# Performance work log

Measured on AMD Instinct MI355X. Metric: run time of the kernel, lower is better.

Reference implementation:

```python
import jax, jax.numpy as jnp
import numpy as np

B, TQ, TK, E, H, DH = 4, 1024, 1024, 1024, 16, 64
EPS = 1e-5

def setup_inputs() -> dict:
    key = jax.random.key(0)
    ks = jax.random.split(key, 16)
    s = 0.02
    return {
        "x": jax.random.normal(ks[0], (B, TQ, E), jnp.float32),
        "encoder_out": jax.random.normal(ks[1], (B, TK, E), jnp.float32),
        "Q1w": jax.random.normal(ks[2], (H, DH, E), jnp.float32) * s,
        "Q1b": jax.random.normal(ks[3], (H, DH), jnp.float32) * s,
        "Q2w": jax.random.normal(ks[4], (H, DH, E), jnp.float32) * s,
        "Q2b": jax.random.normal(ks[5], (H, DH), jnp.float32) * s,
        "K1w": jax.random.normal(ks[6], (H, DH, E), jnp.float32) * s,
        "K1b": jax.random.normal(ks[7], (H, DH), jnp.float32) * s,
        "K2w": jax.random.normal(ks[8], (H, DH, E), jnp.float32) * s,
        "K2b": jax.random.normal(ks[9], (H, DH), jnp.float32) * s,
        "Vw": jax.random.normal(ks[10], (H, DH, E), jnp.float32) * s,
        "Vb": jax.random.normal(ks[11], (H, DH), jnp.float32) * s,
        "lam": jax.random.uniform(ks[12], (H,), jnp.float32, 0.5, 1.0),
        "gn_gamma": jnp.ones((H * DH,), jnp.float32),
        "gn_beta": jnp.zeros((H * DH,), jnp.float32),
        "out_w": jax.random.normal(ks[13], (E, H * DH), jnp.float32) * s,
        "out_b": jax.random.normal(ks[14], (E,), jnp.float32) * s,
    }

def _proj(inp, w, b):
    # inp: [B,T,E], w: [H,DH,E] -> [B,H,T,DH]
    return jnp.einsum('bte,hde->bhtd', inp, w) + b[None, :, None, :]

def reference(x, encoder_out, Q1w, Q1b, Q2w, Q2b, K1w, K1b, K2w, K2b, Vw, Vb,
              lam, gn_gamma, gn_beta, out_w, out_b):
    scale = 1.0 / jnp.sqrt(jnp.float32(DH))
    q1 = _proj(x, Q1w, Q1b)
    q2 = _proj(x, Q2w, Q2b)
    k1 = _proj(encoder_out, K1w, K1b)
    k2 = _proj(encoder_out, K2w, K2b)
    v = _proj(encoder_out, Vw, Vb)
    s1 = jnp.einsum('bhtd,bhsd->bhts', q1, k1) * scale  # [B,H,TQ,TK]
    s2 = jnp.einsum('bhtd,bhsd->bhts', q2, k2) * scale
    w = jax.nn.softmax(s1, axis=-1) - lam[None, :, None, None] * jax.nn.softmax(s2, axis=-1)
    out = jnp.einsum('bhts,bhsd->bhtd', w, v)  # [B,H,TQ,DH]
    # GroupNorm(num_groups=H, channels=H*DH) over [B,C,T]: per (B,H) stats over (T,DH)
    mu = jnp.mean(out, axis=(2, 3), keepdims=True)
    var = jnp.mean(jnp.square(out - mu), axis=(2, 3), keepdims=True)
    normed = (out - mu) * jax.lax.rsqrt(var + EPS)
    g = gn_gamma.reshape(H, DH)[None, :, None, :]
    b_ = gn_beta.reshape(H, DH)[None, :, None, :]
    normed = normed * g + b_
    y = normed.transpose(0, 2, 1, 3).reshape(B, TQ, H * DH)
    return y @ out_w.T + out_b
```

## Files before the change

kernel.cpp:

```cpp
#include <hip/hip_runtime.h>
#include <cmath>

typedef __bf16 bf16_t;
typedef bf16_t bf16x8 __attribute__((ext_vector_type(8)));
typedef bf16_t bf16x4 __attribute__((ext_vector_type(4)));
typedef float  f32x4  __attribute__((ext_vector_type(4)));

#define Bn  4
#define TQn 1024
#define TKn 1024
#define En  1024
#define Hn  16
#define DHn 64

static constexpr float EPSv = 1e-5f;
static constexpr float C_SCALE = 0.18033688011112042f;

#define GLDS16(g, l)                                                         \
    __builtin_amdgcn_global_load_lds(                                        \
        (const __attribute__((address_space(1))) void*)(g),                  \
        (__attribute__((address_space(3))) void*)(l), 16, 0, 0)

__global__ __launch_bounds__(256)
void cvt_all(const float* __restrict__ x, const float* __restrict__ enc,
             const float* __restrict__ q1w, const float* __restrict__ q2w,
             const float* __restrict__ k1w, const float* __restrict__ k2w,
             const float* __restrict__ vw,  const float* __restrict__ outw,
             bf16_t* __restrict__ xb, bf16_t* __restrict__ encb,
             bf16_t* __restrict__ wq, bf16_t* __restrict__ wkv,
             bf16_t* __restrict__ wob, float* __restrict__ stats)
{
    if (blockIdx.x == 0 && threadIdx.x < 128) stats[threadIdx.x] = 0.f;
    int idx = blockIdx.x * 256 + threadIdx.x;
    const float* src; bf16_t* dst;
    if      (idx < 1048576) { src = x    + (size_t)idx * 4;              dst = xb   + (size_t)idx * 4; }
    else if (idx < 2097152) { src = enc  + (size_t)(idx - 1048576) * 4;  dst = encb + (size_t)(idx - 1048576) * 4; }
    else if (idx < 2359296) { src = q1w  + (size_t)(idx - 2097152) * 4;  dst = wq   + (size_t)(idx - 2097152) * 4; }
    else if (idx < 2621440) { src = q2w  + (size_t)(idx - 2359296) * 4;  dst = wq   + 1048576 + (size_t)(idx - 2359296) * 4; }
    else if (idx < 2883584) { src = k1w  + (size_t)(idx - 2621440) * 4;  dst = wkv  + (size_t)(idx - 2621440) * 4; }
    else if (idx < 3145728) { src = k2w  + (size_t)(idx - 2883584) * 4;  dst = wkv  + 1048576 + (size_t)(idx - 2883584) * 4; }
    else if (idx < 3407872) { src = vw   + (size_t)(idx - 3145728) * 4;  dst = wkv  + 2097152 + (size_t)(idx - 3145728) * 4; }
    else                    { src = outw + (size_t)(idx - 3407872) * 4;  dst = wob  + (size_t)(idx - 3407872) * 4; }
    float4 v = *(const float4*)src;
    bf16x4 o;
    o[0] = (bf16_t)v.x; o[1] = (bf16_t)v.y; o[2] = (bf16_t)v.z; o[3] = (bf16_t)v.w;
    *(bf16x4*)dst = o;
}

template<int OUTMODE>
__global__ __launch_bounds__(256, 3)
void gemm_bf16(const bf16_t* __restrict__ A, const bf16_t* __restrict__ W,
               const float* __restrict__ b0, const float* __restrict__ b1,
               const float* __restrict__ b2, void* __restrict__ Cout, int K)
{
    __shared__ bf16_t sA[128 * 64];
    __shared__ bf16_t sB[128 * 64];
    const int tid = threadIdx.x;
    const int w = tid >> 6, lane = tid & 63;
    const int q = lane >> 4, r = lane & 15;
    const int wm = w & 1, wn = w >> 1;
    const int blockM = blockIdx.y * 128, blockN = blockIdx.x * 128;

    f32x4 acc[4][4];
#pragma unroll
    for (int i = 0; i < 4; ++i)
#pragma unroll
        for (int j = 0; j < 4; ++j) acc[i][j] = (f32x4){0.f, 0.f, 0.f, 0.f};

    for (int k0 = 0; k0 < K; k0 += 64) {
#pragma unroll
        for (int c = 0; c < 4; ++c) {
            const int s = c * 256 + tid;
            const int row = s >> 3;
            const int cg = (s & 7) ^ (row & 7);
            GLDS16(A + (size_t)(blockM + row) * K + k0 + cg * 8, sA + c * 2048 + w * 512);
            GLDS16(W + (size_t)(blockN + row) * K + k0 + cg * 8, sB + c * 2048 + w * 512);
        }
        __syncthreads();
#pragma unroll
        for (int ks = 0; ks < 2; ++ks) {
            bf16x8 a[4], b[4];
#pragma unroll
            for (int i = 0; i < 4; ++i) {
                const int row = wm * 64 + i * 16 + r;
                const int g = (ks * 4 + q) ^ (row & 7);
                a[i] = *(const bf16x8*)&sA[row * 64 + g * 8];
            }
#pragma unroll
            for (int j = 0; j < 4; ++j) {
                const int row = wn * 64 + j * 16 + r;
                const int g = (ks * 4 + q) ^ (row & 7);
                b[j] = *(const bf16x8*)&sB[row * 64 + g * 8];
            }
#pragma unroll
            for (int i = 0; i < 4; ++i)
#pragma unroll
                for (int j = 0; j < 4; ++j)
                    acc[i][j] = __builtin_amdgcn_mfma_f32_16x16x32_bf16(a[i], b[j], acc[i][j], 0, 0, 0);
        }
        __syncthreads();
    }

    const int seg = blockN >> 10;
    const float* bp = (seg == 0) ? b0 : ((seg == 1) ? b1 : b2);
#pragma unroll
    for (int j = 0; j < 4; ++j) {
        const int n = blockN + wn * 64 + j * 16 + r;
        const float bv = bp[n & 1023];
#pragma unroll
        for (int i = 0; i < 4; ++i) {
            f32x4 v = acc[i][j];
#pragma unroll
            for (int e = 0; e < 4; ++e) {
                const int m = blockM + wm * 64 + i * 16 + q * 4 + e;
                const float val = v[e] + bv;
                if (OUTMODE == 0) {
                    const int bb = m >> 10, t = m & 1023;
                    const int h = (n >> 6) & 15, d = n & 63;
                    ((bf16_t*)Cout)[((((size_t)seg * 4 + bb) * 16 + h) * 1024 + t) * 64 + d] = (bf16_t)val;
                } else {
                    ((float*)Cout)[(size_t)m * 1024 + n] = val;
                }
            }
        }
    }
}

__device__ __forceinline__ void compute_S(const bf16_t* __restrict__ sK,
                                          const bf16x8 (&fQ)[2][2],
                                          f32x4 (&S)[4][2], int q, int r)
{
#pragma unroll
    for (int i = 0; i < 4; ++i)
#pragma unroll
        for (int j = 0; j < 2; ++j) S[i][j] = (f32x4){0.f, 0.f, 0.f, 0.f};
#pragma unroll
    for (int ks = 0; ks < 2; ++ks) {
        bf16x8 fK[4];
#pragma unroll
        for (int i = 0; i < 4; ++i) {
            const int row = i * 16 + r;
            const int g = (ks * 4 + q) ^ (row & 7);
            fK[i] = *(const bf16x8*)&sK[row * 64 + g * 8];
        }
#pragma unroll
        for (int i = 0; i < 4; ++i)
#pragma unroll
            for (int j = 0; j < 2; ++j)
                S[i][j] = __builtin_amdgcn_mfma_f32_16x16x32_bf16(fK[i], fQ[j][ks], S[i][j], 0, 0, 0);
    }
}

__device__ __forceinline__ void softmax_pw(f32x4 (&S)[4][2], bf16_t* __restrict__ sPt,
                                           float (&l)[2], int w, int q, int r)
{
#pragma unroll
    for (int j = 0; j < 2; ++j) {
        const int t = w * 32 + j * 16 + r;
        float part = 0.f;
#pragma unroll
        for (int i = 0; i < 4; ++i) {
            bf16x4 pk;
#pragma unroll
            for (int e = 0; e < 4; ++e) {
                const float p = __builtin_amdgcn_exp2f(S[i][j][e] * C_SCALE);
                part += p;
                pk[e] = (bf16_t)p;
            }
            const int sb = i * 16 + q * 4;
            const int g = (sb >> 3) ^ (t & 7);
            *(bf16x4*)&sPt[t * 64 + g * 8 + (sb & 7)] = pk;
        }
        l[j] += part;
    }
}

__device__ __forceinline__ void pv(const bf16_t* __restrict__ sPt,
                                   const bf16x8 (&fV)[4][2],
                                   f32x4 (&O)[2][4], int w, int q, int r)
{
#pragma unroll
    for (int ks = 0; ks < 2; ++ks) {
        bf16x8 fP[2];
#pragma unroll
        for (int i2 = 0; i2 < 2; ++i2) {
            const int m = w * 32 + i2 * 16 + r;
            const int g = (ks * 4 + q) ^ (m & 7);
            fP[i2] = *(const bf16x8*)&sPt[m * 64 + g * 8];
        }
#pragma unroll
        for (int i2 = 0; i2 < 2; ++i2)
#pragma unroll
            for (int j = 0; j < 4; ++j)
                O[i2][j] = __builtin_amdgcn_mfma_f32_16x16x32_bf16(fP[i2], fV[j][ks], O[i2][j], 0, 0, 0);
    }
}

__global__ __launch_bounds__(256, 2)
void diff_attn_mfma(const bf16_t* __restrict__ q12, const bf16_t* __restrict__ k12v,
                    const float* __restrict__ lam, bf16_t* __restrict__ out,
                    float* __restrict__ stats)
{
    __shared__ bf16_t sK1[2][64 * 64];
    __shared__ bf16_t sK2[2][64 * 64];
    __shared__ bf16_t sVt[64 * 64];
    __shared__ bf16_t sPt1[128 * 64];
    __shared__ bf16_t sPt2[128 * 64];
    __shared__ float  sl1[128], sl2[128];
    __shared__ float  sred[16];

    const int tid = threadIdx.x;
    const int w = tid >> 6, lane = tid & 63;
    const int q = lane >> 4, r = lane & 15;
    const int bh = blockIdx.x, qt = blockIdx.y;
    const float lamv = lam[bh & (Hn - 1)];

    const size_t HT = (size_t)TKn * DHn;
    const bf16_t* q1g = q12 + (size_t)bh * HT + (size_t)qt * 128 * DHn;
    const bf16_t* q2g = q1g + 64 * HT;
    const bf16_t* k1g = k12v + (size_t)bh * HT;
    const bf16_t* k2g = k1g + 64 * HT;
    const bf16_t* vg  = k1g + 128 * HT;

    bf16x8 fQ1[2][2], fQ2[2][2];
#pragma unroll
    for (int j = 0; j < 2; ++j) {
        const int t = w * 32 + j * 16 + r;
#pragma unroll
        for (int ks = 0; ks < 2; ++ks) {
            fQ1[j][ks] = *(const bf16x8*)(q1g + (size_t)t * 64 + ks * 32 + q * 8);
            fQ2[j][ks] = *(const bf16x8*)(q2g + (size_t)t * 64 + ks * 32 + q * 8);
        }
    }

    f32x4 O1[2][4], O2[2][4];
    float l1[2] = {0.f, 0.f}, l2[2] = {0.f, 0.f};
#pragma unroll
    for (int i = 0; i < 2; ++i)
#pragma unroll
        for (int j = 0; j < 4; ++j) { O1[i][j] = (f32x4){0.f,0.f,0.f,0.f}; O2[i][j] = (f32x4){0.f,0.f,0.f,0.f}; }

    {
#pragma unroll
        for (int c = 0; c < 2; ++c) {
            const int s = c * 256 + tid;
            const int row = s >> 3;
            const int cg = (s & 7) ^ (row & 7);
            GLDS16(k1g + row * 64 + cg * 8, &sK1[0][c * 2048 + w * 512]);
            GLDS16(k2g + row * 64 + cg * 8, &sK2[0][c * 2048 + w * 512]);
        }
        bf16x8 v0[2];
#pragma unroll
        for (int rep = 0; rep < 2; ++rep)
            v0[rep] = *(const bf16x8*)(vg + (size_t)lane * 64 + (w * 2 + rep) * 8);
        __syncthreads();
#pragma unroll
        for (int rep = 0; rep < 2; ++rep) {
            const int d0 = (w * 2 + rep) * 8;
#pragma unroll
            for (int i = 0; i < 8; ++i) {
                const int d = d0 + i;
                sVt[d * 64 + (((lane >> 3) ^ i) << 3) + (lane & 7)] = v0[rep][i];
            }
        }
        __syncthreads();
    }

    bf16x8 vr[2];
    for (int st = 0; st < TKn / 64; ++st) {
        const int cur = st & 1;
        if (st < 15) {
            const bf16_t* k1p = k1g + (size_t)(st + 1) * 4096;
            const bf16_t* k2p = k2g + (size_t)(st + 1) * 4096;
#pragma unroll
            for (int c = 0; c < 2; ++c) {
                const int s = c * 256 + tid;
                const int row = s >> 3;
                const int cg = (s & 7) ^ (row & 7);
                GLDS16(k1p + row * 64 + cg * 8, &sK1[cur ^ 1][c * 2048 + w * 512]);
                GLDS16(k2p + row * 64 + cg * 8, &sK2[cur ^ 1][c * 2048 + w * 512]);
            }
            const bf16_t* vp = vg + (size_t)(st + 1) * 4096;
#pragma unroll
            for (int rep = 0; rep < 2; ++rep)
                vr[rep] = *(const bf16x8*)(vp + (size_t)lane * 64 + (w * 2 + rep) * 8);
        }

        {
            f32x4 S[4][2];
            compute_S(sK1[cur], fQ1, S, q, r);
            softmax_pw(S, sPt1, l1, w, q, r);
        }
        {
            f32x4 S[4][2];
            compute_S(sK2[cur], fQ2, S, q, r);
            softmax_pw(S, sPt2, l2, w, q, r);
        }
        bf16x8 fV[4][2];
#pragma unroll
        for (int j = 0; j < 4; ++j)
#pragma unroll
            for (int ks = 0; ks < 2; ++ks) {
                const int d = j * 16 + r;
                const int g = (ks * 4 + q) ^ (d & 7);
                fV[j][ks] = *(const bf16x8*)&sVt[d * 64 + g * 8];
            }
        pv(sPt1, fV, O1, w, q, r);
        pv(sPt2, fV, O2, w, q, r);

        __syncthreads();
        if (st < 15) {
#pragma unroll
            for (int rep = 0; rep < 2; ++rep) {
                const int d0 = (w * 2 + rep) * 8;
#pragma unroll
                for (int i = 0; i < 8; ++i) {
                    const int d = d0 + i;
                    sVt[d * 64 + (((lane >> 3) ^ i) << 3) + (lane & 7)] = vr[rep][i];
                }
            }
            __syncthreads();
        }
    }

#pragma unroll
    for (int j = 0; j < 2; ++j) {
        float v1 = l1[j];
        v1 += __shfl_xor(v1, 16); v1 += __shfl_xor(v1, 32);
        float v2 = l2[j];
        v2 += __shfl_xor(v2, 16); v2 += __shfl_xor(v2, 32);
        if (q == 0) { sl1[w * 32 + j * 16 + r] = v1; sl2[w * 32 + j * 16 + r] = v2; }
    }

    bf16_t* op = out + ((size_t)bh * TQn + (size_t)qt * 128) * DHn;
    float ssum = 0.f, ssq = 0.f;
#pragma unroll
    for (int i2 = 0; i2 < 2; ++i2)
#pragma unroll
        for (int e = 0; e < 4; ++e) {
            const int t = w * 32 + i2 * 16 + q * 4 + e;
            const float inv1 = 1.0f / sl1[t];
            const float inv2 = lamv / sl2[t];
#pragma unroll
            for (int j = 0; j < 4; ++j) {
                const float o = O1[i2][j][e] * inv1 - O2[i2][j][e] * inv2;
                op[(size_t)t * 64 + j * 16 + r] = (bf16_t)o;
                ssum += o;
                ssq += o * o;
            }
        }
#pragma unroll
    for (int d = 1; d < 64; d <<= 1) {
        ssum += __shfl_xor(ssum, d);
        ssq  += __shfl_xor(ssq, d);
    }
    if (lane == 0) { sred[w] = ssum; sred[8 + w] = ssq; }
    __syncthreads();
    if (tid == 0) {
        atomicAdd(&stats[bh],      sred[0] + sred[1] + sred[2] + sred[3]);
        atomicAdd(&stats[64 + bh], sred[8] + sred[9] + sred[10] + sred[11]);
    }
}

__global__ __launch_bounds__(256)
void gn_apply(const bf16_t* __restrict__ attn, const float* __restrict__ stats,
              const float* __restrict__ gamma, const float* __restrict__ beta,
              bf16_t* __restrict__ y)
{
    const int f = blockIdx.x * 256 + threadIdx.x;
    const int d8 = (f & 7) << 3;
    const int t  = (f >> 3) & 1023;
    const int bh = f >> 13;
    const int h  = bh & 15;
    const int b  = bh >> 4;
    const float s1 = stats[bh], s2 = stats[64 + bh];
    const float mu = s1 * (1.f / 65536.f);
    const float var = s2 * (1.f / 65536.f) - mu * mu;
    const float rstd = rsqrtf(var + EPSv);
    bf16x8 v = *(const bf16x8*)&attn[((size_t)bh << 16) + t * 64 + d8];
    const int c = h * 64 + d8;
    const float* gp = gamma + c;
    const float* bp = beta + c;
    bf16x8 o;
#pragma unroll
    for (int i = 0; i < 8; ++i)
        o[i] = (bf16_t)(((float)v[i] - mu) * rstd * gp[i] + bp[i]);
    *(bf16x8*)&y[((size_t)(b * 1024 + t)) * 1024 + c] = o;
}

extern "C" void kernel_launch(void* const* d_in, const int* in_sizes, int n_in,
                              void* d_out, int out_size, void* d_ws, size_t ws_size,
                              hipStream_t stream)
{
    const float* x    = (const float*)d_in[0];
    const float* enc  = (const float*)d_in[1];
    const float* Q1w  = (const float*)d_in[2];
    const float* Q1b  = (const float*)d_in[3];
    const float* Q2w  = (const float*)d_in[4];
    const float* Q2b  = (const float*)d_in[5];
    const float* K1w  = (const float*)d_in[6];
    const float* K1b  = (const float*)d_in[7];
    const float* K2w  = (const float*)d_in[8];
    const float* K2b  = (const float*)d_in[9];
    const float* Vw   = (const float*)d_in[10];
    const float* Vb   = (const float*)d_in[11];
    const float* lam  = (const float*)d_in[12];
    const float* gng  = (const float*)d_in[13];
    const float* gnb  = (const float*)d_in[14];
    const float* outw = (const float*)d_in[15];
    const float* outb = (const float*)d_in[16];
    float* out = (float*)d_out;

    bf16_t* xb   = (bf16_t*)d_ws;
    bf16_t* encb = xb   + 4194304;
    bf16_t* wq   = encb + 4194304;
    bf16_t* wkv  = wq   + 2097152;
    bf16_t* wob  = wkv  + 3145728;
    bf16_t* q12  = wob  + 1048576;
    bf16_t* k12v = q12  + 8388608;
    bf16_t* yb   = k12v + 12582912;
    bf16_t* attnb= yb   + 4194304;
    float*  stats= (float*)(attnb + 4194304);

    cvt_all<<<14336, 256, 0, stream>>>(x, enc, Q1w, Q2w, K1w, K2w, Vw, outw,
                                       xb, encb, wq, wkv, wob, stats);

    gemm_bf16<0><<<dim3(16, 32), 256, 0, stream>>>(xb,   wq,  Q1b, Q2b, Q2b, q12,  1024);
    gemm_bf16<0><<<dim3(24, 32), 256, 0, stream>>>(encb, wkv, K1b, K2b, Vb,  k12v, 1024);

    diff_attn_mfma<<<dim3(64, 8), 256, 0, stream>>>(q12, k12v, lam, attnb, stats);

    gn_apply<<<2048, 256, 0, stream>>>(attnb, stats, gng, gnb, yb);

    gemm_bf16<1><<<dim3(8, 32), 256, 0, stream>>>(yb, wob, outb, outb, outb, out, 1024);
}
```

Measured before the change: 251.1 us.

## Split attention KV loop across two wave groups and pre-transpose V in GEMM

```diff
diff --git a/kernel.cpp b/kernel.cpp
--- a/kernel.cpp
+++ b/kernel.cpp
@@ -114,10 +114,14 @@
             for (int e = 0; e < 4; ++e) {
                 const int m = blockM + wm * 64 + i * 16 + q * 4 + e;
                 const float val = v[e] + bv;
-                if (OUTMODE == 0) {
+                if (OUTMODE == 0 || OUTMODE == 2) {
                     const int bb = m >> 10, t = m & 1023;
                     const int h = (n >> 6) & 15, d = n & 63;
-                    ((bf16_t*)Cout)[((((size_t)seg * 4 + bb) * 16 + h) * 1024 + t) * 64 + d] = (bf16_t)val;
+                    const size_t base = ((size_t)(seg * 4 + bb) * 16 + h) * 65536;
+                    if (OUTMODE == 2 && seg == 2)
+                        ((bf16_t*)Cout)[base + (size_t)d * 1024 + t] = (bf16_t)val;
+                    else
+                        ((bf16_t*)Cout)[base + (size_t)t * 64 + d] = (bf16_t)val;
                 } else {
                     ((float*)Cout)[(size_t)m * 1024 + n] = val;
                 }
@@ -126,97 +130,27 @@
     }
 }
 
-__device__ __forceinline__ void compute_S(const bf16_t* __restrict__ sK,
-                                          const bf16x8 (&fQ)[2][2],
-                                          f32x4 (&S)[4][2], int q, int r)
-{
-#pragma unroll
-    for (int i = 0; i < 4; ++i)
-#pragma unroll
-        for (int j = 0; j < 2; ++j) S[i][j] = (f32x4){0.f, 0.f, 0.f, 0.f};
-#pragma unroll
-    for (int ks = 0; ks < 2; ++ks) {
-        bf16x8 fK[4];
-#pragma unroll
-        for (int i = 0; i < 4; ++i) {
-            const int row = i * 16 + r;
-            const int g = (ks * 4 + q) ^ (row & 7);
-            fK[i] = *(const bf16x8*)&sK[row * 64 + g * 8];
-        }
-#pragma unroll
-        for (int i = 0; i < 4; ++i)
-#pragma unroll
-            for (int j = 0; j < 2; ++j)
-                S[i][j] = __builtin_amdgcn_mfma_f32_16x16x32_bf16(fK[i], fQ[j][ks], S[i][j], 0, 0, 0);
-    }
-}
-
-__device__ __forceinline__ void softmax_pw(f32x4 (&S)[4][2], bf16_t* __restrict__ sPt,
-                                           float (&l)[2], int w, int q, int r)
-{
-#pragma unroll
-    for (int j = 0; j < 2; ++j) {
-        const int t = w * 32 + j * 16 + r;
-        float part = 0.f;
-#pragma unroll
-        for (int i = 0; i < 4; ++i) {
-            bf16x4 pk;
-#pragma unroll
-            for (int e = 0; e < 4; ++e) {
-                const float p = __builtin_amdgcn_exp2f(S[i][j][e] * C_SCALE);
-                part += p;
-                pk[e] = (bf16_t)p;
-            }
-            const int sb = i * 16 + q * 4;
-            const int g = (sb >> 3) ^ (t & 7);
-            *(bf16x4*)&sPt[t * 64 + g * 8 + (sb & 7)] = pk;
-        }
-        l[j] += part;
-    }
-}
-
-__device__ __forceinline__ void pv(const bf16_t* __restrict__ sPt,
-                                   const bf16x8 (&fV)[4][2],
-                                   f32x4 (&O)[2][4], int w, int q, int r)
-{
-#pragma unroll
-    for (int ks = 0; ks < 2; ++ks) {
-        bf16x8 fP[2];
-#pragma unroll
-        for (int i2 = 0; i2 < 2; ++i2) {
-            const int m = w * 32 + i2 * 16 + r;
-            const int g = (ks * 4 + q) ^ (m & 7);
-            fP[i2] = *(const bf16x8*)&sPt[m * 64 + g * 8];
-        }
-#pragma unroll
-        for (int i2 = 0; i2 < 2; ++i2)
-#pragma unroll
-            for (int j = 0; j < 4; ++j)
-                O[i2][j] = __builtin_amdgcn_mfma_f32_16x16x32_bf16(fP[i2], fV[j][ks], O[i2][j], 0, 0, 0);
-    }
-}
-
-__global__ __launch_bounds__(256, 2)
+__global__ __launch_bounds__(512, 4)
 void diff_attn_mfma(const bf16_t* __restrict__ q12, const bf16_t* __restrict__ k12v,
                     const float* __restrict__ lam, bf16_t* __restrict__ out,
                     float* __restrict__ stats)
 {
-    __shared__ bf16_t sK1[2][64 * 64];
-    __shared__ bf16_t sK2[2][64 * 64];
-    __shared__ bf16_t sVt[64 * 64];
-    __shared__ bf16_t sPt1[128 * 64];
-    __shared__ bf16_t sPt2[128 * 64];
-    __shared__ float  sl1[128], sl2[128];
-    __shared__ float  sred[16];
+    __shared__ __align__(16) bf16_t smem[20480];
 
     const int tid = threadIdx.x;
     const int w = tid >> 6, lane = tid & 63;
+    const int wg = w >> 2, wl = w & 3;
     const int q = lane >> 4, r = lane & 15;
     const int bh = blockIdx.x, qt = blockIdx.y;
     const float lamv = lam[bh & (Hn - 1)];
 
+    bf16_t* sK1 = smem + wg * 2048;
+    bf16_t* sK2 = smem + 4096 + wg * 2048;
+    bf16_t* sVt = smem + 8192 + wg * 2048;
+    bf16_t* sPt = smem + 12288 + w * 1024;
+
     const size_t HT = (size_t)TKn * DHn;
-    const bf16_t* q1g = q12 + (size_t)bh * HT + (size_t)qt * 128 * DHn;
+    const bf16_t* q1g = q12 + (size_t)bh * HT + ((size_t)qt * 128 + wl * 32) * 64;
     const bf16_t* q2g = q1g + 64 * HT;
     const bf16_t* k1g = k12v + (size_t)bh * HT;
     const bf16_t* k2g = k1g + 64 * HT;
@@ -225,11 +159,11 @@
     bf16x8 fQ1[2][2], fQ2[2][2];
 #pragma unroll
     for (int j = 0; j < 2; ++j) {
-        const int t = w * 32 + j * 16 + r;
+        const int t_l = j * 16 + r;
 #pragma unroll
         for (int ks = 0; ks < 2; ++ks) {
-            fQ1[j][ks] = *(const bf16x8*)(q1g + (size_t)t * 64 + ks * 32 + q * 8);
-            fQ2[j][ks] = *(const bf16x8*)(q2g + (size_t)t * 64 + ks * 32 + q * 8);
+            fQ1[j][ks] = *(const bf16x8*)(q1g + (size_t)t_l * 64 + ks * 32 + q * 8);
+            fQ2[j][ks] = *(const bf16x8*)(q2g + (size_t)t_l * 64 + ks * 32 + q * 8);
         }
     }
 
@@ -240,125 +174,157 @@
 #pragma unroll
         for (int j = 0; j < 4; ++j) { O1[i][j] = (f32x4){0.f,0.f,0.f,0.f}; O2[i][j] = (f32x4){0.f,0.f,0.f,0.f}; }
 
-    {
-#pragma unroll
-        for (int c = 0; c < 2; ++c) {
-            const int s = c * 256 + tid;
-            const int row = s >> 3;
-            const int cg = (s & 7) ^ (row & 7);
-            GLDS16(k1g + row * 64 + cg * 8, &sK1[0][c * 2048 + w * 512]);
-            GLDS16(k2g + row * 64 + cg * 8, &sK2[0][c * 2048 + w * 512]);
-        }
-        bf16x8 v0[2];
-#pragma unroll
-        for (int rep = 0; rep < 2; ++rep)
-            v0[rep] = *(const bf16x8*)(vg + (size_t)lane * 64 + (w * 2 + rep) * 8);
+    const int tg = wl * 64 + lane;
+    const int krow = tg >> 3;
+    const int kcg  = (tg & 7) ^ (krow & 7);
+    const int vd  = tg >> 2;
+    const int vcg = (tg & 3) ^ (vd & 3) ^ ((vd >> 2) & 3);
+    const int swzr = (r & 3) ^ ((r >> 2) & 3);
+
+    for (int st = wg; st < 32; st += 2) {
         __syncthreads();
-#pragma unroll
-        for (int rep = 0; rep < 2; ++rep) {
-            const int d0 = (w * 2 + rep) * 8;
-#pragma unroll
-            for (int i = 0; i < 8; ++i) {
-                const int d = d0 + i;
-                sVt[d * 64 + (((lane >> 3) ^ i) << 3) + (lane & 7)] = v0[rep][i];
-            }
-        }
+        GLDS16(k1g + (size_t)st * 2048 + krow * 64 + kcg * 8, sK1 + wl * 512);
+        GLDS16(k2g + (size_t)st * 2048 + krow * 64 + kcg * 8, sK2 + wl * 512);
+        GLDS16(vg + (size_t)vd * 1024 + st * 32 + vcg * 8,    sVt + wl * 512);
         __syncthreads();
-    }
-
-    bf16x8 vr[2];
-    for (int st = 0; st < TKn / 64; ++st) {
-        const int cur = st & 1;
-        if (st < 15) {
-            const bf16_t* k1p = k1g + (size_t)(st + 1) * 4096;
-            const bf16_t* k2p = k2g + (size_t)(st + 1) * 4096;
-#pragma unroll
-            for (int c = 0; c < 2; ++c) {
-                const int s = c * 256 + tid;
-                const int row = s >> 3;
-                const int cg = (s & 7) ^ (row & 7);
-                GLDS16(k1p + row * 64 + cg * 8, &sK1[cur ^ 1][c * 2048 + w * 512]);
-                GLDS16(k2p + row * 64 + cg * 8, &sK2[cur ^ 1][c * 2048 + w * 512]);
-            }
-            const bf16_t* vp = vg + (size_t)(st + 1) * 4096;
-#pragma unroll
-            for (int rep = 0; rep < 2; ++rep)
-                vr[rep] = *(const bf16x8*)(vp + (size_t)lane * 64 + (w * 2 + rep) * 8);
-        }
-
-        {
-            f32x4 S[4][2];
-            compute_S(sK1[cur], fQ1, S, q, r);
-            softmax_pw(S, sPt1, l1, w, q, r);
-        }
-        {
-            f32x4 S[4][2];
-            compute_S(sK2[cur], fQ2, S, q, r);
-            softmax_pw(S, sPt2, l2, w, q, r);
-        }
-        bf16x8 fV[4][2];
-#pragma unroll
-        for (int j = 0; j < 4; ++j)
+
+        bf16x8 fV[4];
+#pragma unroll
+        for (int j = 0; j < 4; ++j) {
+            const int g = q ^ swzr;
+            fV[j] = *(const bf16x8*)&sVt[(j * 16 + r) * 32 + g * 8];
+        }
+
+#pragma unroll
+        for (int stream = 0; stream < 2; ++stream) {
+            const bf16_t* sK = stream ? sK2 : sK1;
+            const bf16x8 (&fQ)[2][2] = stream ? fQ2 : fQ1;
+            float* lp = stream ? l2 : l1;
+            f32x4 (&O)[2][4] = stream ? O2 : O1;
+
+            f32x4 S[2][2];
+#pragma unroll
+            for (int i = 0; i < 2; ++i)
+#pragma unroll
+                for (int j = 0; j < 2; ++j) S[i][j] = (f32x4){0.f,0.f,0.f,0.f};
 #pragma unroll
             for (int ks = 0; ks < 2; ++ks) {
-                const int d = j * 16 + r;
-                const int g = (ks * 4 + q) ^ (d & 7);
-                fV[j][ks] = *(const bf16x8*)&sVt[d * 64 + g * 8];
-            }
-        pv(sPt1, fV, O1, w, q, r);
-        pv(sPt2, fV, O2, w, q, r);
-
-        __syncthreads();
-        if (st < 15) {
-#pragma unroll
-            for (int rep = 0; rep < 2; ++rep) {
-                const int d0 = (w * 2 + rep) * 8;
-#pragma unroll
-                for (int i = 0; i < 8; ++i) {
-                    const int d = d0 + i;
-                    sVt[d * 64 + (((lane >> 3) ^ i) << 3) + (lane & 7)] = vr[rep][i];
+                bf16x8 fK[2];
+#pragma unroll
+                for (int i = 0; i < 2; ++i) {
+                    const int g = (ks * 4 + q) ^ (r & 7);
+                    fK[i] = *(const bf16x8*)&sK[(i * 16 + r) * 64 + g * 8];
                 }
-            }
-            __syncthreads();
-        }
-    }
-
-#pragma unroll
-    for (int j = 0; j < 2; ++j) {
-        float v1 = l1[j];
-        v1 += __shfl_xor(v1, 16); v1 += __shfl_xor(v1, 32);
-        float v2 = l2[j];
-        v2 += __shfl_xor(v2, 16); v2 += __shfl_xor(v2, 32);
-        if (q == 0) { sl1[w * 32 + j * 16 + r] = v1; sl2[w * 32 + j * 16 + r] = v2; }
-    }
-
-    bf16_t* op = out + ((size_t)bh * TQn + (size_t)qt * 128) * DHn;
-    float ssum = 0.f, ssq = 0.f;
-#pragma unroll
-    for (int i2 = 0; i2 < 2; ++i2)
-#pragma unroll
-        for (int e = 0; e < 4; ++e) {
-            const int t = w * 32 + i2 * 16 + q * 4 + e;
-            const float inv1 = 1.0f / sl1[t];
-            const float inv2 = lamv / sl2[t];
-#pragma unroll
-            for (int j = 0; j < 4; ++j) {
-                const float o = O1[i2][j][e] * inv1 - O2[i2][j][e] * inv2;
-                op[(size_t)t * 64 + j * 16 + r] = (bf16_t)o;
-                ssum += o;
-                ssq += o * o;
-            }
-        }
-#pragma unroll
-    for (int d = 1; d < 64; d <<= 1) {
-        ssum += __shfl_xor(ssum, d);
-        ssq  += __shfl_xor(ssq, d);
-    }
-    if (lane == 0) { sred[w] = ssum; sred[8 + w] = ssq; }
+#pragma unroll
+                for (int i = 0; i < 2; ++i)
+#pragma unroll
+                    for (int j = 0; j < 2; ++j)
+                        S[i][j] = __builtin_amdgcn_mfma_f32_16x16x32_bf16(fK[i], fQ[j][ks], S[i][j], 0, 0, 0);
+            }
+#pragma unroll
+            for (int j = 0; j < 2; ++j) {
+                const int t_l = j * 16 + r;
+                float part = 0.f;
+#pragma unroll
+                for (int i = 0; i < 2; ++i) {
+                    bf16x4 pk;
+#pragma unroll
+                    for (int e = 0; e < 4; ++e) {
+                        const float p = __builtin_amdgcn_exp2f(S[i][j][e] * C_SCALE);
+                        part += p;
+                        pk[e] = (bf16_t)p;
+                    }
+                    const int sg = i * 2 + (q >> 1);
+                    const int g = sg ^ swzr;
+                    *(bf16x4*)&sPt[t_l * 32 + g * 8 + (q & 1) * 4] = pk;
+                }
+                lp[j] += part;
+            }
+            bf16x8 fP[2];
+#pragma unroll
+            for (int i2 = 0; i2 < 2; ++i2) {
+                const int g = q ^ swzr;
+                fP[i2] = *(const bf16x8*)&sPt[(i2 * 16 + r) * 32 + g * 8];
+            }
+#pragma unroll
+            for (int i2 = 0; i2 < 2; ++i2)
+#pragma unroll
+                for (int j = 0; j < 4; ++j)
+                    O[i2][j] = __builtin_amdgcn_mfma_f32_16x16x32_bf16(fP[i2], fV[j], O[i2][j], 0, 0, 0);
+        }
+    }
+
+    float* scr = (float*)smem;
+    const int li = wl * 64 + lane;
     __syncthreads();
-    if (tid == 0) {
-        atomicAdd(&stats[bh],      sred[0] + sred[1] + sred[2] + sred[3]);
-        atomicAdd(&stats[64 + bh], sred[8] + sred[9] + sred[10] + sred[11]);
+    if (wg == 1) {
+#pragma unroll
+        for (int i2 = 0; i2 < 2; ++i2)
+#pragma unroll
+            for (int j = 0; j < 4; ++j)
+                *(f32x4*)&scr[li * 32 + (i2 * 4 + j) * 4] = O1[i2][j];
+        f32x4 lv = {l1[0], l1[1], l2[0], l2[1]};
+        *(f32x4*)&scr[8192 + li * 4] = lv;
+    }
+    __syncthreads();
+    if (wg == 0) {
+#pragma unroll
+        for (int i2 = 0; i2 < 2; ++i2)
+#pragma unroll
+            for (int j = 0; j < 4; ++j)
+                O1[i2][j] += *(const f32x4*)&scr[li * 32 + (i2 * 4 + j) * 4];
+        f32x4 lv = *(const f32x4*)&scr[8192 + li * 4];
+        l1[0] += lv[0]; l1[1] += lv[1]; l2[0] += lv[2]; l2[1] += lv[3];
+    }
+    __syncthreads();
+    if (wg == 1) {
+#pragma unroll
+        for (int i2 = 0; i2 < 2; ++i2)
+#pragma unroll
+            for (int j = 0; j < 4; ++j)
+                *(f32x4*)&scr[li * 32 + (i2 * 4 + j) * 4] = O2[i2][j];
+    }
+    __syncthreads();
+    if (wg == 0) {
+#pragma unroll
+        for (int i2 = 0; i2 < 2; ++i2)
+#pragma unroll
+            for (int j = 0; j < 4; ++j)
+                O2[i2][j] += *(const f32x4*)&scr[li * 32 + (i2 * 4 + j) * 4];
+
+#pragma unroll
+        for (int j = 0; j < 2; ++j) {
+            l1[j] += __shfl_xor(l1[j], 16); l1[j] += __shfl_xor(l1[j], 32);
+            l2[j] += __shfl_xor(l2[j], 16); l2[j] += __shfl_xor(l2[j], 32);
+        }
+
+        bf16_t* op = out + ((size_t)bh * TQn + (size_t)qt * 128 + wl * 32) * DHn;
+        float ssum = 0.f, ssq = 0.f;
+#pragma unroll
+        for (int i2 = 0; i2 < 2; ++i2)
+#pragma unroll
+            for (int e = 0; e < 4; ++e) {
+                const int rr = q * 4 + e;
+                const float inv1 = 1.0f / __shfl(l1[i2], rr);
+                const float inv2 = lamv / __shfl(l2[i2], rr);
+                const int t_l = i2 * 16 + rr;
+#pragma unroll
+                for (int j = 0; j < 4; ++j) {
+                    const float o = O1[i2][j][e] * inv1 - O2[i2][j][e] * inv2;
+                    op[(size_t)t_l * 64 + j * 16 + r] = (bf16_t)o;
+                    ssum += o;
+                    ssq += o * o;
+                }
+            }
+#pragma unroll
+        for (int d = 1; d < 64; d <<= 1) {
+            ssum += __shfl_xor(ssum, d);
+            ssq  += __shfl_xor(ssq, d);
+        }
+        if (lane == 0) {
+            atomicAdd(&stats[bh], ssum);
+            atomicAdd(&stats[64 + bh], ssq);
+        }
     }
 }
 
@@ -426,9 +392,9 @@
                                        xb, encb, wq, wkv, wob, stats);
 
     gemm_bf16<0><<<dim3(16, 32), 256, 0, stream>>>(xb,   wq,  Q1b, Q2b, Q2b, q12,  1024);
-    gemm_bf16<0><<<dim3(24, 32), 256, 0, stream>>>(encb, wkv, K1b, K2b, Vb,  k12v, 1024);
-
-    diff_attn_mfma<<<dim3(64, 8), 256, 0, stream>>>(q12, k12v, lam, attnb, stats);
+    gemm_bf16<2><<<dim3(24, 32), 256, 0, stream>>>(encb, wkv, K1b, K2b, Vb,  k12v, 1024);
+
+    diff_attn_mfma<<<dim3(64, 8), 512, 0, stream>>>(q12, k12v, lam, attnb, stats);
 
     gn_apply<<<2048, 256, 0, stream>>>(attnb, stats, gng, gnb, yb);
 
```

Result: slower. 322.1 us (+28.3%).
